# Kernel tuning notes

Measured on AMD Instinct MI355X. Metric: run time of the kernel, lower is better.

The kernel has to match this reference:

```python
import jax, jax.numpy as jnp
import numpy as np

# ---- model constants (match init_kwargs) ----
B, N, T, L = 16384, 32, 300, 1
DIM = 2                      # len(state_index)
DT = 1.0 / (T * L)           # dt = 1/(T*l)
STEPS = T * L                # Euler integration steps (time_steps = STEPS+1)
A_X = 1.0                    # canonical DMP phase constant
TAU = 1.0
HID = 64
OUT = N * DIM + DIM          # fc2_mean output size


def setup_inputs() -> dict:
    key = jax.random.key(0)
    ks = jax.random.split(key, 8)
    s = lambda i, shape, scale: jax.random.normal(ks[i], shape, jnp.float32) * scale
    inp = {
        "state": jax.random.normal(ks[0], (B, 3), jnp.float32),
        "fc1_w": s(1, (HID, 3), 0.3),
        "fc1_b": jnp.full((HID,), 0.1, jnp.float32),
        "fc2m_w": s(2, (OUT, HID), 0.1),
        "fc2m_b": jnp.full((OUT,), 0.1, jnp.float32),
        "sig_w": s(3, (DIM, HID), 0.1),
        "sig_b": jnp.zeros((DIM,), jnp.float32),
        "val_w": s(4, (DIM, HID), 0.1),
        "val_b": jnp.zeros((DIM,), jnp.float32),
    }
    # DMPParameters: gaussian RBF centers on exp-decayed phase, canonical widths
    c = jnp.exp(-A_X * jnp.linspace(0.0, 1.0, N))
    inp["dmp_c"] = c.astype(jnp.float32)
    inp["dmp_sigma2"] = (N ** 1.5 / c / A_X).astype(jnp.float32)
    return inp


def dmp_rollout(w, goal, y0, dy0, a_z, c, sigma2):
    """Euler rollout of DMP transformation system.
    w: [M,N] basis weights, goal/y0/dy0/a_z: [M] per-channel scalars.
    Returns Y, dY, ddY each [M, STEPS+1]."""
    z0 = dy0 * TAU
    b_z = a_z / 4.0

    def step(carry, _):
        x, y, z = carry
        x = x + (-A_X * x) * TAU * DT                       # phase update
        psi = jnp.exp(-0.5 * (x - c) ** 2 / sigma2)          # [N] gaussian RBF
        fx = (w @ psi) * x * (goal - y0) / jnp.sum(psi)      # [M] forcing term
        dz = a_z * (b_z * (goal - y) - z) + fx
        dy = z
        y = y + TAU * dy * DT
        z = z + TAU * dz * DT
        return (x, y, z), (y, dy * TAU, dz * TAU)

    _, (Ys, dYs, ddYs) = jax.lax.scan(
        step, (jnp.float32(1.0), y0, z0), None, length=STEPS)
    Y = jnp.concatenate([y0[None], Ys], axis=0).T            # [M, STEPS+1]
    dY = jnp.concatenate([dy0[None], dYs], axis=0).T
    ddY = jnp.concatenate([z0[None], ddYs], axis=0).T
    return Y, dY, ddY


def reference(state, fc1_w, fc1_b, fc2m_w, fc2m_b, sig_w, sig_b,
              val_w, val_b, dmp_c, dmp_sigma2):
    x = jnp.tanh(state @ fc1_w.T + fc1_b) * 0.1              # [B,64]
    y0 = state[:, :DIM].reshape(-1)                           # [M=B*DIM]
    dy0 = jnp.zeros_like(y0) + 0.01

    # value = fc2_value(x).repeat(1,T).view(-1,T,2).transpose(1,2) == broadcast over T
    v = x @ val_w.T + val_b                                   # [B,2]
    value = jnp.broadcast_to(v[:, :, None], (B, DIM, T))

    sigma = (jax.nn.sigmoid(x @ sig_w.T + sig_b) * 1.0 + 0.001).reshape(-1, DIM, 1)

    ndp_wg = x @ fc2m_w.T + fc2m_b                            # [B, 2N+2]
    goal = ndp_wg[:, :DIM].reshape(-1)                        # [M]
    w = ndp_wg[:, DIM:DIM * (N + 1)].reshape(-1, N)           # [M,N]
    a_z = jnp.clip(ndp_wg[:, -1], 0.5, 30.0)                  # learned a_z (az=True)
    a_z = jnp.broadcast_to(a_z[:, None], (B, DIM)).reshape(-1)

    Y, _, _ = dmp_rollout(w, goal, y0, dy0, a_z, dmp_c, dmp_sigma2)
    y = Y.reshape(B, DIM, -1)[:, :, ::L]                      # [B,2,T+1]
    a = y[:, :, 1:] - y[:, :, :-1]                            # [B,2,T]
    return (a, sigma, value)
```

## Files before the change

kernel.cpp:

```cpp
#include <hip/hip_runtime.h>
#include <hip/hip_bf16.h>

#define NB 32
#define TS 300
#define NBATCH 16384
#define DTF (1.0f/300.0f)
#define A_ELEMS (NBATCH*2*TS)

typedef __attribute__((ext_vector_type(8))) short bf16x8;
typedef __attribute__((ext_vector_type(4))) float f32x4;

static __device__ __forceinline__ ushort f2bf(float f) {
    union { __hip_bfloat16 h; ushort u; } cv;
    cv.h = __float2bfloat16(f);
    return cv.u;
}


__global__ __launch_bounds__(1024) void k_prep(
    const float* __restrict__ fc2m_w, const float* __restrict__ fc2m_b,
    const float* __restrict__ sig_w, const float* __restrict__ sig_b,
    const float* __restrict__ val_w, const float* __restrict__ val_b,
    const float* __restrict__ dmp_c, const float* __restrict__ dmp_s2,
    uint4* __restrict__ wsPhi, uint4* __restrict__ wsB,
    float* __restrict__ wsBias)
{
    const int t = threadIdx.x;
    if (t < 304) {
        ushort row[NB];
        if (t < TS) {
            const float x = exp2f((float)(t + 1) * log2f(1.0f - DTF));
            float ps[NB]; float s = 0.0f;
            #pragma unroll
            for (int n = 0; n < NB; ++n) {
                float d = x - dmp_c[n];
                float p = __expf(-0.5f * d * d / dmp_s2[n]);
                ps[n] = p; s += p;
            }
            const float inv = x / s;
            #pragma unroll
            for (int n = 0; n < NB; ++n) row[n] = f2bf(ps[n] * inv);
        } else {
            #pragma unroll
            for (int n = 0; n < NB; ++n) row[n] = 0;
        }
        #pragma unroll
        for (int g0 = 0; g0 < 4; ++g0) {
            union { ushort us[8]; uint4 v; } pk;
            #pragma unroll
            for (int e = 0; e < 8; ++e) pk.us[e] = row[g0*8 + e];
            wsPhi[(t >> 4)*64 + g0*16 + (t & 15)] = pk.v;
        }
    } else if (t < 944) {
        const int e = t - 304;
        const int T = e >> 7, kk = (e >> 6) & 1, lane = e & 63;
        const int r = T*16 + (lane & 15);
        const int k0 = kk*32 + (lane >> 4)*8;
        union { ushort us[8]; uint4 v; } pk;
        if (r < 70) {
            const float* src = (r < 66) ? (fc2m_w + r*64 + k0)
                             : (r < 68) ? (sig_w + (r-66)*64 + k0)
                             : (val_w + (r-68)*64 + k0);
            #pragma unroll
            for (int i = 0; i < 8; ++i) pk.us[i] = f2bf(src[i]);
        } else {
            #pragma unroll
            for (int i = 0; i < 8; ++i) pk.us[i] = 0;
        }
        wsB[e] = pk.v;
    } else {
        const int r = t - 944;
        wsBias[r] = (r < 66) ? fc2m_b[r] : (r < 68) ? sig_b[r-66]
                  : (r < 70) ? val_b[r-68] : 0.0f;
    }
}

__global__ __launch_bounds__(256) void k_head(
    const float* __restrict__ state,
    const float* __restrict__ fc1_w, const float* __restrict__ fc1_b,
    const uint4* __restrict__ wsB, const float* __restrict__ wsBias,
    float* __restrict__ sig_out, float* __restrict__ pbuf,
    ushort* __restrict__ wbuf16)
{
    __shared__ float f1[64*4];
    __shared__ float biasl[80];
    __shared__ float hlds[4*16*68];
    __shared__ float ct[4*16*84];

    const int tid = threadIdx.x;
    const int wv  = tid >> 6;
    const int l   = tid & 63;
    const int b16 = l & 15;
    const int g   = l >> 4;

    if (tid < 64) {
        f1[tid*4+0] = fc1_w[tid*3+0];
        f1[tid*4+1] = fc1_w[tid*3+1];
        f1[tid*4+2] = fc1_w[tid*3+2];
        f1[tid*4+3] = fc1_b[tid];
    }
    if (tid < 80) biasl[tid] = wsBias[tid];
    __syncthreads();

    const int bbase = blockIdx.x*64 + wv*16;
    const int bglob = bbase + b16;
    const float s0 = state[bglob*3+0], s1 = state[bglob*3+1], s2 = state[bglob*3+2];

    float* hrow = hlds + wv*1088 + b16*68;
    #pragma unroll
    for (int i = 0; i < 16; ++i) {
        const int hid = g + 4*i;
        const float4 fw = *(const float4*)(f1 + hid*4);
        const float pre = fmaf(fw.x, s0, fmaf(fw.y, s1, fmaf(fw.z, s2, fw.w)));
        const float e = __expf(2.0f * pre);
        hrow[hid] = (1.0f - 2.0f/(e + 1.0f)) * 0.1f;
    }

    bf16x8 A0, A1;
    {
        const float* hr = hlds + wv*1088 + b16*68 + g*8;
        const float4 h0 = *(const float4*)(hr),     h1 = *(const float4*)(hr + 4);
        const float4 h2 = *(const float4*)(hr + 32), h3 = *(const float4*)(hr + 36);
        union { bf16x8 v; ushort u[8]; } p0, p1;
        p0.u[0]=f2bf(h0.x); p0.u[1]=f2bf(h0.y); p0.u[2]=f2bf(h0.z); p0.u[3]=f2bf(h0.w);
        p0.u[4]=f2bf(h1.x); p0.u[5]=f2bf(h1.y); p0.u[6]=f2bf(h1.z); p0.u[7]=f2bf(h1.w);
        p1.u[0]=f2bf(h2.x); p1.u[1]=f2bf(h2.y); p1.u[2]=f2bf(h2.z); p1.u[3]=f2bf(h2.w);
        p1.u[4]=f2bf(h3.x); p1.u[5]=f2bf(h3.y); p1.u[6]=f2bf(h3.z); p1.u[7]=f2bf(h3.w);
        A0 = p0.v; A1 = p1.v;
    }

    float* ctw = ct + wv*1344;
    const f32x4 zacc = {0.0f, 0.0f, 0.0f, 0.0f};
    #pragma unroll
    for (int T = 0; T < 5; ++T) {
        union { uint4 q; bf16x8 v; } B0, B1;
        B0.q = wsB[(T*2+0)*64 + l];
        B1.q = wsB[(T*2+1)*64 + l];
        f32x4 acc = __builtin_amdgcn_mfma_f32_16x16x32_bf16(A0, B0.v, zacc, 0, 0, 0);
        acc = __builtin_amdgcn_mfma_f32_16x16x32_bf16(A1, B1.v, acc, 0, 0, 0);
        const int r = T*16 + b16;
        const float bs = biasl[r];
        #pragma unroll
        for (int reg = 0; reg < 4; ++reg)
            ctw[(g*4 + reg)*84 + r] = acc[reg] + bs;
    }

    uint* wout = (uint*)wbuf16;
    #pragma unroll 1
    for (int b = 0; b < 16; ++b) {
        if (l < 32) {
            const float2 wp = *(const float2*)(ctw + b*84 + 2 + 2*l);
            wout[(bbase + b)*32 + l] = (uint)f2bf(wp.x) | ((uint)f2bf(wp.y) << 16);
        }
    }
    if (l < 16) {
        const float* cb = ctw + l*84;
        const float goal = cb[0];
        const float az = fminf(fmaxf(cb[65], 0.5f), 30.0f);
        const float y0 = state[(bbase + l)*3 + 0];
        *(float4*)(pbuf + ((bbase + l)*2 + 0)*4) = make_float4(goal, goal - y0, az, cb[68]);
    } else if (l < 32) {
        const int b = l - 16;
        const float* cb = ctw + b*84;
        const float goal = cb[1];
        const float az = fminf(fmaxf(cb[65], 0.5f), 30.0f);
        const float y0 = state[(bbase + b)*3 + 1];
        *(float4*)(pbuf + ((bbase + b)*2 + 1)*4) = make_float4(goal, goal - y0, az, cb[69]);
    } else if (l < 48) {
        const int b = l - 32;
        const float* cb = ctw + b*84;
        const float sg0 = 1.0f / (1.0f + __expf(-cb[66])) + 0.001f;
        const float sg1 = 1.0f / (1.0f + __expf(-cb[67])) + 0.001f;
        *(float2*)(sig_out + (bbase + b)*2) = make_float2(sg0, sg1);
    }
}

__global__ __launch_bounds__(256) void k_roll(
    const uint4* __restrict__ wsPhi, const float* __restrict__ pbuf,
    const ushort* __restrict__ wbuf16, float* __restrict__ a_out,
    float* __restrict__ v_out)
{
    __shared__ float4 xt[4][16][5];
    const int tid = threadIdx.x;
    const int wv = tid >> 6;
    const int j  = tid & 63;
    const int ch = j & 15;
    const int g  = j >> 4;
    const int m  = (blockIdx.x << 6) + (wv << 4) + ch;

    const float4 pp = *(const float4*)(pbuf + m*4);
    const float az = pp.z;
    const float Ac = DTF * az * az * 0.25f;
    const float Kc = DTF * pp.y;
    const float c0 = Ac * pp.x;
    const float OmB = 1.0f - DTF * az;
    float y = pp.x - pp.y;
    float z = 0.01f;

    const bf16x8 wb = *(const bf16x8*)(wbuf16 + m*NB + g*8);
    const bf16x8* ap = (const bf16x8*)wsPhi;
    bf16x8 af = ap[j];

    const int mloc = j >> 2;
    const int m_st = (blockIdx.x << 6) + (wv << 4) + mloc;
    float* aptr = a_out + m_st*TS + (j & 3)*4;
    float* vptr = v_out + m_st*TS + (j & 3)*4;
    const bool tail_ok = (j & 3) < 3;
    float4 vsp;
    {
        const float fv = pbuf[((blockIdx.x << 6) + (wv << 4) + mloc)*4 + 3];
        vsp = make_float4(fv, fv, fv, fv);
    }

    const f32x4 zacc = {0.0f, 0.0f, 0.0f, 0.0f};

    for (int c = 0; c < 19; ++c) {
        f32x4 facc = __builtin_amdgcn_mfma_f32_16x16x32_bf16(af, wb, zacc, 0, 0, 0);
        if (c < 18) af = ap[(c + 1)*64 + j];

        float F[16];
        #pragma unroll
        for (int q = 0; q < 4; ++q) {
            float a = facc[q], b = facc[q];
            asm volatile("v_permlane16_swap_b32 %0, %1" : "+v"(a), "+v"(b));
            float a2 = a, b2 = b;
            asm volatile("v_permlane32_swap_b32 %0, %1" : "+v"(a), "+v"(a2));
            asm volatile("v_permlane32_swap_b32 %0, %1" : "+v"(b), "+v"(b2));
            F[0*4+q] = a; F[1*4+q] = b; F[2*4+q] = a2; F[3*4+q] = b2;
        }

        float avq[4] = {0.f, 0.f, 0.f, 0.f};
        #pragma unroll
        for (int i = 0; i < 16; ++i) {
            const float aval = z * DTF;
            if (g == (i >> 2)) avq[i & 3] = aval;
            float t2 = fmaf(Kc, F[i], c0);
            t2 = fmaf(-Ac, y, t2);
            z = fmaf(OmB, z, t2);
            y += aval;
        }

        xt[wv][ch][g] = make_float4(avq[0], avq[1], avq[2], avq[3]);
        if (c < 18 || tail_ok) {
            const float4 s4 = xt[wv][mloc][j & 3];
            *(float4*)aptr = s4;
            *(float4*)vptr = vsp;
        }
        aptr += 16; vptr += 16;
    }
}

extern "C" void kernel_launch(void* const* d_in, const int* in_sizes, int n_in,
                              void* d_out, int out_size, void* d_ws, size_t ws_size,
                              hipStream_t stream) {
    (void)in_sizes; (void)n_in; (void)out_size; (void)ws_size;
    const float* state  = (const float*)d_in[0];
    const float* fc1_w  = (const float*)d_in[1];
    const float* fc1_b  = (const float*)d_in[2];
    const float* fc2m_w = (const float*)d_in[3];
    const float* fc2m_b = (const float*)d_in[4];
    const float* sig_w  = (const float*)d_in[5];
    const float* sig_b  = (const float*)d_in[6];
    const float* val_w  = (const float*)d_in[7];
    const float* val_b  = (const float*)d_in[8];
    const float* dmp_c  = (const float*)d_in[9];
    const float* dmp_s2 = (const float*)d_in[10];

    float* out     = (float*)d_out;
    float* a_out   = out;
    float* sig_out = out + A_ELEMS;
    float* v_out   = out + A_ELEMS + NBATCH*2;

    char* ws = (char*)d_ws;
    uint4*  wsPhi  = (uint4*)ws;
    uint4*  wsB    = (uint4*)(ws + 19456);
    float*  wsBias = (float*)(ws + 29696);
    float*  pbuf   = (float*)(ws + 32768);
    ushort* wbuf16 = (ushort*)(ws + 557056);

    k_prep<<<dim3(1), dim3(1024), 0, stream>>>(fc2m_w, fc2m_b, sig_w, sig_b,
                                               val_w, val_b, dmp_c, dmp_s2,
                                               wsPhi, wsB, wsBias);
    k_head<<<dim3(256), dim3(256), 0, stream>>>(state, fc1_w, fc1_b, wsB, wsBias,
                                                sig_out, pbuf, wbuf16);
    k_roll<<<dim3(512), dim3(256), 0, stream>>>(wsPhi, pbuf, wbuf16, a_out, v_out);
}
```

Baseline: 33.31 us.

## Fuse prep into head kernel, fold scaling into weights, double-buffer rollout stores

Removes the single-block prep kernel by having each head block build the bf16 weight tiles in shared memory, with an extra block computing the RBF basis table. This saves one launch and a serial dependency. The forcing-term scale DT*(goal-y0) is folded into the bf16 basis weights and the constant term is seeded into the MFMA accumulator, which shortens the rollout inner recurrence. The action transpose buffer is double-buffered so the store for one chunk is issued after the next chunk's compute, and the value stores move ahead of the MFMA. Costs are redundant per-block weight conversion and slightly different bf16 rounding, since the scale is now applied before quantisation.

```diff
diff --git a/kernel.cpp b/kernel.cpp
--- a/kernel.cpp
+++ b/kernel.cpp
@@ -17,42 +17,61 @@
 }
 
 
-__global__ __launch_bounds__(1024) void k_prep(
+__global__ __launch_bounds__(256) void k_head(
+    const float* __restrict__ state,
+    const float* __restrict__ fc1_w, const float* __restrict__ fc1_b,
     const float* __restrict__ fc2m_w, const float* __restrict__ fc2m_b,
     const float* __restrict__ sig_w, const float* __restrict__ sig_b,
     const float* __restrict__ val_w, const float* __restrict__ val_b,
     const float* __restrict__ dmp_c, const float* __restrict__ dmp_s2,
-    uint4* __restrict__ wsPhi, uint4* __restrict__ wsB,
-    float* __restrict__ wsBias)
+    float* __restrict__ sig_out, float* __restrict__ pbuf,
+    ushort* __restrict__ wbuf16, uint4* __restrict__ wsPhi)
 {
-    const int t = threadIdx.x;
-    if (t < 304) {
-        ushort row[NB];
-        if (t < TS) {
-            const float x = exp2f((float)(t + 1) * log2f(1.0f - DTF));
-            float ps[NB]; float s = 0.0f;
+    const int tid = threadIdx.x;
+    if (blockIdx.x == 256) {
+        const float l2 = log2f(1.0f - DTF);
+        for (int t = tid; t < 304; t += 256) {
+            ushort row[NB];
+            if (t < TS) {
+                const float x = exp2f((float)(t + 1) * l2);
+                float ps[NB]; float s = 0.0f;
+                #pragma unroll
+                for (int n = 0; n < NB; ++n) {
+                    float d = x - dmp_c[n];
+                    float p = __expf(-0.5f * d * d / dmp_s2[n]);
+                    ps[n] = p; s += p;
+                }
+                const float inv = x / s;
+                #pragma unroll
+                for (int n = 0; n < NB; ++n) row[n] = f2bf(ps[n] * inv);
+            } else {
+                #pragma unroll
+                for (int n = 0; n < NB; ++n) row[n] = 0;
+            }
             #pragma unroll
-            for (int n = 0; n < NB; ++n) {
-                float d = x - dmp_c[n];
-                float p = __expf(-0.5f * d * d / dmp_s2[n]);
-                ps[n] = p; s += p;
+            for (int g0 = 0; g0 < 4; ++g0) {
+                union { ushort us[8]; uint4 v; } pk;
+                #pragma unroll
+                for (int e = 0; e < 8; ++e) pk.us[e] = row[g0*8 + e];
+                wsPhi[(t >> 4)*64 + g0*16 + (t & 15)] = pk.v;
             }
-            const float inv = x / s;
-            #pragma unroll
-            for (int n = 0; n < NB; ++n) row[n] = f2bf(ps[n] * inv);
-        } else {
-            #pragma unroll
-            for (int n = 0; n < NB; ++n) row[n] = 0;
-        }
-        #pragma unroll
-        for (int g0 = 0; g0 < 4; ++g0) {
-            union { ushort us[8]; uint4 v; } pk;
-            #pragma unroll
-            for (int e = 0; e < 8; ++e) pk.us[e] = row[g0*8 + e];
-            wsPhi[(t >> 4)*64 + g0*16 + (t & 15)] = pk.v;
-        }
-    } else if (t < 944) {
-        const int e = t - 304;
+        }
+        return;
+    }
+
+    __shared__ uint4 bfr[640];
+    __shared__ float f1s[64*4];
+    __shared__ float biasl[80];
+    __shared__ float hlds[4*16*68];
+    __shared__ float ct[4*16*84];
+    __shared__ float scl[4][16][2];
+
+    const int wv  = tid >> 6;
+    const int l   = tid & 63;
+    const int b16 = l & 15;
+    const int g   = l >> 4;
+
+    for (int e = tid; e < 640; e += 256) {
         const int T = e >> 7, kk = (e >> 6) & 1, lane = e & 63;
         const int r = T*16 + (lane & 15);
         const int k0 = kk*32 + (lane >> 4)*8;
@@ -67,39 +86,16 @@
             #pragma unroll
             for (int i = 0; i < 8; ++i) pk.us[i] = 0;
         }
-        wsB[e] = pk.v;
-    } else {
-        const int r = t - 944;
-        wsBias[r] = (r < 66) ? fc2m_b[r] : (r < 68) ? sig_b[r-66]
-                  : (r < 70) ? val_b[r-68] : 0.0f;
-    }
-}
-
-__global__ __launch_bounds__(256) void k_head(
-    const float* __restrict__ state,
-    const float* __restrict__ fc1_w, const float* __restrict__ fc1_b,
-    const uint4* __restrict__ wsB, const float* __restrict__ wsBias,
-    float* __restrict__ sig_out, float* __restrict__ pbuf,
-    ushort* __restrict__ wbuf16)
-{
-    __shared__ float f1[64*4];
-    __shared__ float biasl[80];
-    __shared__ float hlds[4*16*68];
-    __shared__ float ct[4*16*84];
-
-    const int tid = threadIdx.x;
-    const int wv  = tid >> 6;
-    const int l   = tid & 63;
-    const int b16 = l & 15;
-    const int g   = l >> 4;
-
+        bfr[e] = pk.v;
+    }
     if (tid < 64) {
-        f1[tid*4+0] = fc1_w[tid*3+0];
-        f1[tid*4+1] = fc1_w[tid*3+1];
-        f1[tid*4+2] = fc1_w[tid*3+2];
-        f1[tid*4+3] = fc1_b[tid];
-    }
-    if (tid < 80) biasl[tid] = wsBias[tid];
+        f1s[tid*4+0] = fc1_w[tid*3+0];
+        f1s[tid*4+1] = fc1_w[tid*3+1];
+        f1s[tid*4+2] = fc1_w[tid*3+2];
+        f1s[tid*4+3] = fc1_b[tid];
+    }
+    if (tid < 80) biasl[tid] = (tid < 66) ? fc2m_b[tid] : (tid < 68) ? sig_b[tid-66]
+                             : (tid < 70) ? val_b[tid-68] : 0.0f;
     __syncthreads();
 
     const int bbase = blockIdx.x*64 + wv*16;
@@ -110,7 +106,7 @@
     #pragma unroll
     for (int i = 0; i < 16; ++i) {
         const int hid = g + 4*i;
-        const float4 fw = *(const float4*)(f1 + hid*4);
+        const float4 fw = *(const float4*)(f1s + hid*4);
         const float pre = fmaf(fw.x, s0, fmaf(fw.y, s1, fmaf(fw.z, s2, fw.w)));
         const float e = __expf(2.0f * pre);
         hrow[hid] = (1.0f - 2.0f/(e + 1.0f)) * 0.1f;
@@ -119,7 +115,7 @@
     bf16x8 A0, A1;
     {
         const float* hr = hlds + wv*1088 + b16*68 + g*8;
-        const float4 h0 = *(const float4*)(hr),     h1 = *(const float4*)(hr + 4);
+        const float4 h0 = *(const float4*)(hr),      h1 = *(const float4*)(hr + 4);
         const float4 h2 = *(const float4*)(hr + 32), h3 = *(const float4*)(hr + 36);
         union { bf16x8 v; ushort u[8]; } p0, p1;
         p0.u[0]=f2bf(h0.x); p0.u[1]=f2bf(h0.y); p0.u[2]=f2bf(h0.z); p0.u[3]=f2bf(h0.w);
@@ -134,8 +130,8 @@
     #pragma unroll
     for (int T = 0; T < 5; ++T) {
         union { uint4 q; bf16x8 v; } B0, B1;
-        B0.q = wsB[(T*2+0)*64 + l];
-        B1.q = wsB[(T*2+1)*64 + l];
+        B0.q = bfr[(T*2+0)*64 + l];
+        B1.q = bfr[(T*2+1)*64 + l];
         f32x4 acc = __builtin_amdgcn_mfma_f32_16x16x32_bf16(A0, B0.v, zacc, 0, 0, 0);
         acc = __builtin_amdgcn_mfma_f32_16x16x32_bf16(A1, B1.v, acc, 0, 0, 0);
         const int r = T*16 + b16;
@@ -145,27 +141,34 @@
             ctw[(g*4 + reg)*84 + r] = acc[reg] + bs;
     }
 
+    if (l < 32) {
+        const int b = l & 15, d = l >> 4;
+        const float goal = ctw[b*84 + d];
+        const float y0 = state[(bbase + b)*3 + d];
+        scl[wv][b][d] = DTF * (goal - y0);
+    }
+
     uint* wout = (uint*)wbuf16;
     #pragma unroll 1
     for (int b = 0; b < 16; ++b) {
         if (l < 32) {
             const float2 wp = *(const float2*)(ctw + b*84 + 2 + 2*l);
-            wout[(bbase + b)*32 + l] = (uint)f2bf(wp.x) | ((uint)f2bf(wp.y) << 16);
+            const float sc = scl[wv][b][l >> 4];
+            wout[(bbase + b)*32 + l] =
+                (uint)f2bf(wp.x * sc) | ((uint)f2bf(wp.y * sc) << 16);
         }
     }
     if (l < 16) {
         const float* cb = ctw + l*84;
-        const float goal = cb[0];
         const float az = fminf(fmaxf(cb[65], 0.5f), 30.0f);
         const float y0 = state[(bbase + l)*3 + 0];
-        *(float4*)(pbuf + ((bbase + l)*2 + 0)*4) = make_float4(goal, goal - y0, az, cb[68]);
+        *(float4*)(pbuf + ((bbase + l)*2 + 0)*4) = make_float4(cb[0], az, y0, cb[68]);
     } else if (l < 32) {
         const int b = l - 16;
         const float* cb = ctw + b*84;
-        const float goal = cb[1];
         const float az = fminf(fmaxf(cb[65], 0.5f), 30.0f);
         const float y0 = state[(bbase + b)*3 + 1];
-        *(float4*)(pbuf + ((bbase + b)*2 + 1)*4) = make_float4(goal, goal - y0, az, cb[69]);
+        *(float4*)(pbuf + ((bbase + b)*2 + 1)*4) = make_float4(cb[1], az, y0, cb[69]);
     } else if (l < 48) {
         const int b = l - 32;
         const float* cb = ctw + b*84;
@@ -180,7 +183,7 @@
     const ushort* __restrict__ wbuf16, float* __restrict__ a_out,
     float* __restrict__ v_out)
 {
-    __shared__ float4 xt[4][16][5];
+    __shared__ float4 xt[2][4][16][5];
     const int tid = threadIdx.x;
     const int wv = tid >> 6;
     const int j  = tid & 63;
@@ -189,13 +192,13 @@
     const int m  = (blockIdx.x << 6) + (wv << 4) + ch;
 
     const float4 pp = *(const float4*)(pbuf + m*4);
-    const float az = pp.z;
-    const float Ac = DTF * az * az * 0.25f;
-    const float Kc = DTF * pp.y;
+    const float az = pp.y;
+    const float Ac = (DTF * 0.25f) * az * az;
+    const float OmB = fmaf(-DTF, az, 1.0f);
     const float c0 = Ac * pp.x;
-    const float OmB = 1.0f - DTF * az;
-    float y = pp.x - pp.y;
+    float y = pp.z;
     float z = 0.01f;
+    const f32x4 cvec = {c0, c0, c0, c0};
 
     const bf16x8 wb = *(const bf16x8*)(wbuf16 + m*NB + g*8);
     const bf16x8* ap = (const bf16x8*)wsPhi;
@@ -208,14 +211,15 @@
     const bool tail_ok = (j & 3) < 3;
     float4 vsp;
     {
-        const float fv = pbuf[((blockIdx.x << 6) + (wv << 4) + mloc)*4 + 3];
+        const float fv = pbuf[m_st*4 + 3];
         vsp = make_float4(fv, fv, fv, fv);
     }
 
-    const f32x4 zacc = {0.0f, 0.0f, 0.0f, 0.0f};
-
     for (int c = 0; c < 19; ++c) {
-        f32x4 facc = __builtin_amdgcn_mfma_f32_16x16x32_bf16(af, wb, zacc, 0, 0, 0);
+        if (c < 18 || tail_ok) { *(float4*)vptr = vsp; }
+        vptr += 16;
+
+        f32x4 facc = __builtin_amdgcn_mfma_f32_16x16x32_bf16(af, wb, cvec, 0, 0, 0);
         if (c < 18) af = ap[(c + 1)*64 + j];
 
         float F[16];
@@ -232,21 +236,22 @@
         float avq[4] = {0.f, 0.f, 0.f, 0.f};
         #pragma unroll
         for (int i = 0; i < 16; ++i) {
-            const float aval = z * DTF;
-            if (g == (i >> 2)) avq[i & 3] = aval;
-            float t2 = fmaf(Kc, F[i], c0);
-            t2 = fmaf(-Ac, y, t2);
+            const float t2 = fmaf(-Ac, y, F[i]);
+            if (g == (i >> 2)) avq[i & 3] = z;
+            y = fmaf(DTF, z, y);
             z = fmaf(OmB, z, t2);
-            y += aval;
-        }
-
-        xt[wv][ch][g] = make_float4(avq[0], avq[1], avq[2], avq[3]);
-        if (c < 18 || tail_ok) {
-            const float4 s4 = xt[wv][mloc][j & 3];
-            *(float4*)aptr = s4;
-            *(float4*)vptr = vsp;
-        }
-        aptr += 16; vptr += 16;
+        }
+
+        if (c > 0) {
+            const float4 xs = xt[(c - 1) & 1][wv][mloc][j & 3];
+            *(float4*)aptr = make_float4(xs.x*DTF, xs.y*DTF, xs.z*DTF, xs.w*DTF);
+            aptr += 16;
+        }
+        xt[c & 1][wv][ch][g] = make_float4(avq[0], avq[1], avq[2], avq[3]);
+    }
+    if (tail_ok) {
+        const float4 xs = xt[0][wv][mloc][j & 3];
+        *(float4*)aptr = make_float4(xs.x*DTF, xs.y*DTF, xs.z*DTF, xs.w*DTF);
     }
 }
 
@@ -273,15 +278,12 @@
 
     char* ws = (char*)d_ws;
     uint4*  wsPhi  = (uint4*)ws;
-    uint4*  wsB    = (uint4*)(ws + 19456);
-    float*  wsBias = (float*)(ws + 29696);
     float*  pbuf   = (float*)(ws + 32768);
     ushort* wbuf16 = (ushort*)(ws + 557056);
 
-    k_prep<<<dim3(1), dim3(1024), 0, stream>>>(fc2m_w, fc2m_b, sig_w, sig_b,
-                                               val_w, val_b, dmp_c, dmp_s2,
-                                               wsPhi, wsB, wsBias);
-    k_head<<<dim3(256), dim3(256), 0, stream>>>(state, fc1_w, fc1_b, wsB, wsBias,
-                                                sig_out, pbuf, wbuf16);
+    k_head<<<dim3(257), dim3(256), 0, stream>>>(state, fc1_w, fc1_b, fc2m_w, fc2m_b,
+                                                sig_w, sig_b, val_w, val_b,
+                                                dmp_c, dmp_s2,
+                                                sig_out, pbuf, wbuf16, wsPhi);
     k_roll<<<dim3(512), dim3(256), 0, stream>>>(wsPhi, pbuf, wbuf16, a_out, v_out);
 }
```

Result: faster. 30.63 us (-8.0%).
